# Kernel optimization log

Hardware: AMD Instinct MI355X
Metric: run time of the kernel (lower is better)

The kernel has to match this reference:

```python
import jax, jax.numpy as jnp
import numpy as np
import math

B, S, D = 2, 2048, 1024
H, DK = 16, 64
NUM_BUCKETS = 32
MAX_DISTANCE = 128


def setup_inputs() -> dict:
    key = jax.random.key(0)
    ks = jax.random.split(key, 6)
    scale = 1.0 / math.sqrt(D)
    return {
        "hidden_states": jax.random.normal(ks[0], (B, S, D), jnp.float32),
        "wq": jax.random.normal(ks[1], (D, H * DK), jnp.float32) * scale,
        "wk": jax.random.normal(ks[2], (D, H * DK), jnp.float32) * scale,
        "wv": jax.random.normal(ks[3], (D, H * DK), jnp.float32) * scale,
        "wo": jax.random.normal(ks[4], (H * DK, D), jnp.float32) * scale,
        "rel_bias": jax.random.normal(ks[5], (NUM_BUCKETS, H), jnp.float32),
    }


def _relative_position_bucket(relative_position):
    # Encoder (bidirectional) bucketing, matching T5/UMT5.
    num_buckets = NUM_BUCKETS // 2  # 16
    relative_buckets = (relative_position > 0).astype(jnp.int32) * num_buckets
    relative_position = jnp.abs(relative_position)
    max_exact = num_buckets // 2  # 8
    is_small = relative_position < max_exact
    rp_f = jnp.maximum(relative_position.astype(jnp.float32), 1.0)  # avoid log(0); masked by is_small
    log_ratio = jnp.log(rp_f / max_exact) / math.log(MAX_DISTANCE / max_exact)
    rp_large = max_exact + (log_ratio * (num_buckets - max_exact)).astype(jnp.int32)
    rp_large = jnp.minimum(rp_large, num_buckets - 1)
    return relative_buckets + jnp.where(is_small, relative_position, rp_large)


def compute_bias(query_length, key_length, rel_bias):
    ctx = jnp.arange(query_length)[:, None]
    mem = jnp.arange(key_length)[None, :]
    buckets = _relative_position_bucket(mem - ctx)  # [Sq, Sk]
    values = rel_bias[buckets]                       # [Sq, Sk, H]
    return jnp.transpose(values, (2, 0, 1))[None]    # [1, H, Sq, Sk]


def reference(hidden_states, wq, wk, wv, wo, rel_bias):
    b, s, _ = hidden_states.shape
    q = (hidden_states @ wq).reshape(b, s, H, DK).transpose(0, 2, 1, 3)  # [B,H,S,DK]
    k = (hidden_states @ wk).reshape(b, s, H, DK).transpose(0, 2, 1, 3)
    v = (hidden_states @ wv).reshape(b, s, H, DK).transpose(0, 2, 1, 3)
    scores = jnp.einsum("bhqd,bhkd->bhqk", q, k)  # no 1/sqrt(d) scaling (T5 style)
    scores = scores + compute_bias(s, s, rel_bias)
    attn = jax.nn.softmax(scores.astype(jnp.float32), axis=-1).astype(scores.dtype)
    ctx = jnp.einsum("bhqk,bhkd->bhqd", attn, v)
    ctx = ctx.transpose(0, 2, 1, 3).reshape(b, s, H * DK)
    attn_output = ctx @ wo
    return attn_output, attn
```

## Files before the change

### kernel.cpp

```cpp
#include <hip/hip_runtime.h>

typedef __attribute__((ext_vector_type(8))) short bf16x8;
typedef __attribute__((ext_vector_type(4))) float f32x4;

#define MFMA16 __builtin_amdgcn_mfma_f32_16x16x32_bf16

__device__ __forceinline__ float fexp2(float x) {
#if __has_builtin(__builtin_amdgcn_exp2f)
    return __builtin_amdgcn_exp2f(x);
#else
    return __expf(x * 0.6931471805599453f);
#endif
}

__device__ __forceinline__ short f2bf(float f) {
    union { float f; unsigned u; } v; v.f = f;
    unsigned r = v.u + 0x7fffu + ((v.u >> 16) & 1u);
    return (short)(r >> 16);
}

__device__ __forceinline__ void gl_lds16(const short* g, short* l) {
    __builtin_amdgcn_global_load_lds(
        (const __attribute__((address_space(1))) unsigned int*)g,
        (__attribute__((address_space(3))) unsigned int*)l, 16, 0, 0);
}

__global__ __launch_bounds__(256) void cast_hidden(const float* __restrict__ src,
                                                   short* __restrict__ dst, int n) {
    int i = (blockIdx.x * 256 + threadIdx.x) * 4;
    if (i < n) {
        float4 f = *(const float4*)(src + i);
        short4 o = make_short4(f2bf(f.x), f2bf(f.y), f2bf(f.z), f2bf(f.w));
        *(short4*)(dst + i) = o;
    }
}

__global__ __launch_bounds__(256) void transpose_cast(const float* __restrict__ src,
                                                      short* __restrict__ dst) {
    __shared__ float tile[32][33];
    int tx = threadIdx.x, ty = threadIdx.y;
    int bx = blockIdx.x * 32, by = blockIdx.y * 32;
#pragma unroll
    for (int i = 0; i < 4; ++i)
        tile[ty + i * 8][tx] = src[(size_t)(by + ty + i * 8) * 1024 + bx + tx];
    __syncthreads();
#pragma unroll
    for (int i = 0; i < 4; ++i)
        dst[(size_t)(bx + ty + i * 8) * 1024 + by + tx] = f2bf(tile[tx][ty + i * 8]);
}

__global__ __launch_bounds__(256) void build_bias(const float* __restrict__ relb,
                                                  float* __restrict__ tab) {
    int d = blockIdx.x * 256 + threadIdx.x;
    if (d < 4095) {
        int rel = d - 2047;
        int rp = rel < 0 ? -rel : rel;
        int bucket;
        if (rp < 8)
            bucket = rp;
        else
            bucket = 8 + (rp >= 12) + (rp >= 16) + (rp >= 23) + (rp >= 32) +
                     (rp >= 46) + (rp >= 64) + (rp >= 91);
        if (rel > 0) bucket += 16;
#pragma unroll
        for (int hh = 0; hh < 16; ++hh)
            tab[hh * 4095 + d] = relb[bucket * 16 + hh] * 1.4426950408889634f;
    }
}

__global__ __launch_bounds__(256) void gemm128(const short* __restrict__ A,
                                               const short* __restrict__ BT, int Kdim,
                                               int mode, short* __restrict__ qb,
                                               short* __restrict__ kb,
                                               short* __restrict__ vtb,
                                               float* __restrict__ fout) {
    __shared__ short As[128 * 32];
    __shared__ short Bs[128 * 32];
    const int tid = threadIdx.x, wave = tid >> 6, lane = tid & 63;
    const int quad = lane >> 4, col = lane & 15;
    const int wm = wave >> 1, wn = wave & 1;
    const int m0 = blockIdx.x * 128, n0 = blockIdx.y * 128;

    f32x4 zero4 = {0.f, 0.f, 0.f, 0.f};
    f32x4 acc[4][4];
#pragma unroll
    for (int i = 0; i < 4; ++i)
#pragma unroll
        for (int j = 0; j < 4; ++j) acc[i][j] = zero4;

    const int nk = Kdim >> 5;
    for (int kk = 0; kk < nk; ++kk) {
        __syncthreads();
#pragma unroll
        for (int c = 0; c < 2; ++c) {
            int L = c * 256 + wave * 64 + lane;
            int row = L >> 2, c4 = L & 3;
            int gc = c4 ^ ((row >> 1) & 3);
            gl_lds16(A + (size_t)(m0 + row) * Kdim + kk * 32 + gc * 8,
                     &As[(c * 256 + wave * 64) * 8]);
            gl_lds16(BT + (size_t)(n0 + row) * Kdim + kk * 32 + gc * 8,
                     &Bs[(c * 256 + wave * 64) * 8]);
        }
        __syncthreads();
        bf16x8 af[4], bfr[4];
#pragma unroll
        for (int i = 0; i < 4; ++i) {
            int ra = wm * 64 + i * 16 + col;
            af[i] = *(const bf16x8*)(&As[ra * 32 + (quad ^ ((ra >> 1) & 3)) * 8]);
            int rb = wn * 64 + i * 16 + col;
            bfr[i] = *(const bf16x8*)(&Bs[rb * 32 + (quad ^ ((rb >> 1) & 3)) * 8]);
        }
#pragma unroll
        for (int mi = 0; mi < 4; ++mi)
#pragma unroll
            for (int ni = 0; ni < 4; ++ni)
                acc[mi][ni] = MFMA16(af[mi], bfr[ni], acc[mi][ni], 0, 0, 0);
    }

#pragma unroll
    for (int mi = 0; mi < 4; ++mi) {
#pragma unroll
        for (int ni = 0; ni < 4; ++ni) {
#pragma unroll
            for (int r = 0; r < 4; ++r) {
                int gm = m0 + wm * 64 + mi * 16 + quad * 4 + r;
                int gn = n0 + wn * 64 + ni * 16 + col;
                float v = acc[mi][ni][r];
                if (mode == 1) {
                    fout[(size_t)gm * 1024 + gn] = v;
                } else {
                    int widx = gn >> 10, nn = gn & 1023;
                    int hh = nn >> 6, dk = nn & 63;
                    int bb = gm >> 11, ss = gm & 2047;
                    size_t bh = (size_t)(bb * 16 + hh);
                    if (widx == 0)
                        qb[(bh * 2048 + ss) * 64 + dk] = f2bf(v);
                    else if (widx == 1)
                        kb[(bh * 2048 + ss) * 64 + dk] = f2bf(v);
                    else
                        vtb[(bh * 64 + dk) * 2048 + ss] = f2bf(v);
                }
            }
        }
    }
}

__global__ __launch_bounds__(256) void attn_kernel(const short* __restrict__ qbuf,
                                                   const short* __restrict__ kbuf,
                                                   const short* __restrict__ vtbuf,
                                                   const float* __restrict__ bias_tab,
                                                   float* __restrict__ attn_out,
                                                   short* __restrict__ ctxbuf) {
    __shared__ short Ks[128 * 64];
    __shared__ short Vts[64 * 128];
    __shared__ short Pt[4][640];

    const int tid = threadIdx.x;
    const int wave = tid >> 6, lane = tid & 63;
    const int quad = lane >> 4, col = lane & 15;

    const int raw = blockIdx.x;
    const int blk = (raw & 7) * 128 + (raw >> 3);
    const int qt = blk & 31, h = (blk >> 5) & 15, b = blk >> 9;
    const int q0 = qt * 64 + wave * 16;

    const size_t bh = (size_t)(b * 16 + h);
    const short* Kh = kbuf + bh * 2048 * 64;
    const short* VTh = vtbuf + bh * 64 * 2048;
    const short* Qh = qbuf + bh * 2048 * 64;
    const float* btab = bias_tab + h * 4095;
    const float L2E = 1.4426950408889634f;

    bf16x8 aq0 = *(const bf16x8*)(Qh + (q0 + col) * 64 + quad * 8);
    bf16x8 aq1 = *(const bf16x8*)(Qh + (q0 + col) * 64 + 32 + quad * 8);

    float m = -1e30f, l = 0.f;

    {
#pragma unroll
        for (int c = 0; c < 4; ++c) {
            int L = c * 256 + wave * 64 + lane;
            int row = L >> 3, gc = (L & 7) ^ (row & 7);
            gl_lds16(Kh + (size_t)row * 64 + gc * 8, &Ks[(c * 256 + wave * 64) * 8]);
        }
        for (int kt = 0; kt < 16; ++kt) {
            __syncthreads();
            short* cur = (kt & 1) ? Vts : Ks;
            if (kt < 15) {
                short* nxt = (kt & 1) ? Ks : Vts;
#pragma unroll
                for (int c = 0; c < 4; ++c) {
                    int L = c * 256 + wave * 64 + lane;
                    int row = L >> 3, gc = (L & 7) ^ (row & 7);
                    gl_lds16(Kh + (size_t)((kt + 1) * 128 + row) * 64 + gc * 8,
                             &nxt[(c * 256 + wave * 64) * 8]);
                }
            }
            const float* bp = btab + (kt * 128 - (q0 + col) + 2047 + quad * 4);
            float sv[32];
            __builtin_amdgcn_s_setprio(1);
#pragma unroll
            for (int st = 0; st < 8; ++st) {
                f32x4 acc = {0.f, 0.f, 0.f, 0.f};
                int krow = st * 16 + col;
                bf16x8 bk0 = *(const bf16x8*)(&cur[krow * 64 + (quad ^ (krow & 7)) * 8]);
                bf16x8 bk1 = *(const bf16x8*)(&cur[krow * 64 + ((4 + quad) ^ (krow & 7)) * 8]);
                acc = MFMA16(bk0, aq0, acc, 0, 0, 0);
                acc = MFMA16(bk1, aq1, acc, 0, 0, 0);
#pragma unroll
                for (int r = 0; r < 4; ++r)
                    sv[st * 4 + r] = fmaf(acc[r], L2E, bp[st * 16 + r]);
            }
            __builtin_amdgcn_s_setprio(0);
            float tm = sv[0];
#pragma unroll
            for (int i = 1; i < 32; ++i) tm = fmaxf(tm, sv[i]);
            float mn = fmaxf(m, tm);
            float sum = 0.f;
#pragma unroll
            for (int i = 0; i < 32; ++i) sum += fexp2(sv[i] - mn);
            l = l * fexp2(m - mn) + sum;
            m = mn;
        }
    }
#pragma unroll
    for (int off = 16; off < 64; off <<= 1) {
        float mo = __shfl_xor(m, off);
        float lo = __shfl_xor(l, off);
        float mn = fmaxf(m, mo);
        l = l * fexp2(m - mn) + lo * fexp2(mo - mn);
        m = mn;
    }
    const float moff = m + __log2f(l);

    f32x4 zero4 = {0.f, 0.f, 0.f, 0.f};
    f32x4 ctx[4];
#pragma unroll
    for (int dt = 0; dt < 4; ++dt) ctx[dt] = zero4;

    for (int kt = 0; kt < 16; ++kt) {
        __syncthreads();
#pragma unroll
        for (int c = 0; c < 4; ++c) {
            int L = c * 256 + wave * 64 + lane;
            int row = L >> 3, gc = (L & 7) ^ (row & 7);
            gl_lds16(Kh + (size_t)(kt * 128 + row) * 64 + gc * 8,
                     &Ks[(c * 256 + wave * 64) * 8]);
        }
#pragma unroll
        for (int c = 0; c < 4; ++c) {
            int L = c * 256 + wave * 64 + lane;
            int row = L >> 4, gc = (L & 15) ^ (row & 7);
            gl_lds16(VTh + (size_t)row * 2048 + kt * 128 + gc * 8,
                     &Vts[(c * 256 + wave * 64) * 8]);
        }
        __syncthreads();
        const float* bp = btab + (kt * 128 - (q0 + col) + 2047 + quad * 4);
        float* aout = attn_out + ((bh * 2048 + q0 + col) * 2048 + kt * 128 + quad * 4);
        __builtin_amdgcn_s_setprio(1);
#pragma unroll
        for (int pr = 0; pr < 4; ++pr) {
#pragma unroll
            for (int hf = 0; hf < 2; ++hf) {
                int st = pr * 2 + hf;
                f32x4 acc = {0.f, 0.f, 0.f, 0.f};
                int krow = st * 16 + col;
                bf16x8 bk0 = *(const bf16x8*)(&Ks[krow * 64 + (quad ^ (krow & 7)) * 8]);
                bf16x8 bk1 = *(const bf16x8*)(&Ks[krow * 64 + ((4 + quad) ^ (krow & 7)) * 8]);
                acc = MFMA16(bk0, aq0, acc, 0, 0, 0);
                acc = MFMA16(bk1, aq1, acc, 0, 0, 0);
                f32x4 pv;
                short4 pb;
#pragma unroll
                for (int r = 0; r < 4; ++r) {
                    float p = fexp2(fmaf(acc[r], L2E, bp[st * 16 + r]) - moff);
                    pv[r] = p;
                    ((short*)&pb)[r] = f2bf(p);
                }
                __builtin_nontemporal_store(pv, (f32x4*)(aout + st * 16));
                *(short4*)(&Pt[wave][col * 40 + hf * 16 + quad * 4]) = pb;
            }
            bf16x8 ap = *(const bf16x8*)(&Pt[wave][col * 40 + quad * 8]);
#pragma unroll
            for (int dt = 0; dt < 4; ++dt) {
                int vrow = dt * 16 + col;
                bf16x8 bv = *(const bf16x8*)(&Vts[vrow * 128 + ((pr * 4 + quad) ^ (vrow & 7)) * 8]);
                ctx[dt] = MFMA16(ap, bv, ctx[dt], 0, 0, 0);
            }
        }
        __builtin_amdgcn_s_setprio(0);
    }
#pragma unroll
    for (int dt = 0; dt < 4; ++dt)
#pragma unroll
        for (int r = 0; r < 4; ++r) {
            int q = q0 + quad * 4 + r;
            ctxbuf[((size_t)(b * 2048 + q)) * 1024 + h * 64 + dt * 16 + col] =
                f2bf(ctx[dt][r]);
        }
}

extern "C" void kernel_launch(void* const* d_in, const int* in_sizes, int n_in,
                              void* d_out, int out_size, void* d_ws, size_t ws_size,
                              hipStream_t stream) {
    const float* hs = (const float*)d_in[0];
    const float* wq = (const float*)d_in[1];
    const float* wk = (const float*)d_in[2];
    const float* wv = (const float*)d_in[3];
    const float* wo = (const float*)d_in[4];
    const float* rb = (const float*)d_in[5];
    float* out = (float*)d_out;

    char* ws = (char*)d_ws;
    short* hsb  = (short*)(ws);
    short* wt   = (short*)(ws + ((size_t)8 << 20));
    short* wot  = (short*)(ws + ((size_t)14 << 20));
    short* qb   = (short*)(ws + ((size_t)16 << 20));
    short* kb   = (short*)(ws + ((size_t)24 << 20));
    short* vtb  = (short*)(ws + ((size_t)32 << 20));
    short* ctxb = (short*)(ws + ((size_t)40 << 20));
    float* btab = (float*)(ws + ((size_t)48 << 20));

    cast_hidden<<<4096, 256, 0, stream>>>(hs, hsb, 4096 * 1024);
    dim3 tb(32, 8);
    transpose_cast<<<dim3(32, 32), tb, 0, stream>>>(wq, wt);
    transpose_cast<<<dim3(32, 32), tb, 0, stream>>>(wk, wt + (1u << 20));
    transpose_cast<<<dim3(32, 32), tb, 0, stream>>>(wv, wt + (2u << 20));
    transpose_cast<<<dim3(32, 32), tb, 0, stream>>>(wo, wot);
    build_bias<<<16, 256, 0, stream>>>(rb, btab);

    gemm128<<<dim3(32, 24), 256, 0, stream>>>(hsb, wt, 1024, 0, qb, kb, vtb, nullptr);
    attn_kernel<<<1024, 256, 0, stream>>>(qb, kb, vtb, btab, out + 4194304, ctxb);
    gemm128<<<dim3(32, 8), 256, 0, stream>>>(ctxb, wot, 1024, 1, nullptr, nullptr, nullptr, out);
}
```

Before: 795.1 us.

## Read K/V directly from global memory and drop running-max softmax pass

Removes the LDS staging of K and V^T tiles, including the double-buffered async loads and block barriers. Each wave now loads its MFMA operands straight from global memory and relies on the cache for reuse. The first pass also drops the online max tracking and accumulates exp2 sums without subtracting a max. That saves the max reduction and rescaling, but it can overflow if scores get large. Direct global loads cost more memory traffic and latency in exchange for no synchronisation.

```diff
diff --git a/kernel.cpp b/kernel.cpp
--- a/kernel.cpp
+++ b/kernel.cpp
@@ -151,8 +151,6 @@
                                                    const float* __restrict__ bias_tab,
                                                    float* __restrict__ attn_out,
                                                    short* __restrict__ ctxbuf) {
-    __shared__ short Ks[128 * 64];
-    __shared__ short Vts[64 * 128];
     __shared__ short Pt[4][640];
 
     const int tid = threadIdx.x;
@@ -174,64 +172,26 @@
     bf16x8 aq0 = *(const bf16x8*)(Qh + (q0 + col) * 64 + quad * 8);
     bf16x8 aq1 = *(const bf16x8*)(Qh + (q0 + col) * 64 + 32 + quad * 8);
 
-    float m = -1e30f, l = 0.f;
-
-    {
-#pragma unroll
-        for (int c = 0; c < 4; ++c) {
-            int L = c * 256 + wave * 64 + lane;
-            int row = L >> 3, gc = (L & 7) ^ (row & 7);
-            gl_lds16(Kh + (size_t)row * 64 + gc * 8, &Ks[(c * 256 + wave * 64) * 8]);
-        }
-        for (int kt = 0; kt < 16; ++kt) {
-            __syncthreads();
-            short* cur = (kt & 1) ? Vts : Ks;
-            if (kt < 15) {
-                short* nxt = (kt & 1) ? Ks : Vts;
-#pragma unroll
-                for (int c = 0; c < 4; ++c) {
-                    int L = c * 256 + wave * 64 + lane;
-                    int row = L >> 3, gc = (L & 7) ^ (row & 7);
-                    gl_lds16(Kh + (size_t)((kt + 1) * 128 + row) * 64 + gc * 8,
-                             &nxt[(c * 256 + wave * 64) * 8]);
-                }
-            }
-            const float* bp = btab + (kt * 128 - (q0 + col) + 2047 + quad * 4);
-            float sv[32];
-            __builtin_amdgcn_s_setprio(1);
-#pragma unroll
-            for (int st = 0; st < 8; ++st) {
-                f32x4 acc = {0.f, 0.f, 0.f, 0.f};
-                int krow = st * 16 + col;
-                bf16x8 bk0 = *(const bf16x8*)(&cur[krow * 64 + (quad ^ (krow & 7)) * 8]);
-                bf16x8 bk1 = *(const bf16x8*)(&cur[krow * 64 + ((4 + quad) ^ (krow & 7)) * 8]);
-                acc = MFMA16(bk0, aq0, acc, 0, 0, 0);
-                acc = MFMA16(bk1, aq1, acc, 0, 0, 0);
-#pragma unroll
-                for (int r = 0; r < 4; ++r)
-                    sv[st * 4 + r] = fmaf(acc[r], L2E, bp[st * 16 + r]);
-            }
-            __builtin_amdgcn_s_setprio(0);
-            float tm = sv[0];
-#pragma unroll
-            for (int i = 1; i < 32; ++i) tm = fmaxf(tm, sv[i]);
-            float mn = fmaxf(m, tm);
-            float sum = 0.f;
-#pragma unroll
-            for (int i = 0; i < 32; ++i) sum += fexp2(sv[i] - mn);
-            l = l * fexp2(m - mn) + sum;
-            m = mn;
-        }
-    }
-#pragma unroll
-    for (int off = 16; off < 64; off <<= 1) {
-        float mo = __shfl_xor(m, off);
-        float lo = __shfl_xor(l, off);
-        float mn = fmaxf(m, mo);
-        l = l * fexp2(m - mn) + lo * fexp2(mo - mn);
-        m = mn;
-    }
-    const float moff = m + __log2f(l);
+    float l = 0.f;
+    for (int kt = 0; kt < 16; ++kt) {
+        const short* Kt = Kh + kt * 128 * 64;
+        const float* bp = btab + (kt * 128 - (q0 + col) + 2047 + quad * 4);
+#pragma unroll
+        for (int st = 0; st < 8; ++st) {
+            int krow = st * 16 + col;
+            bf16x8 bk0 = *(const bf16x8*)(Kt + krow * 64 + quad * 8);
+            bf16x8 bk1 = *(const bf16x8*)(Kt + krow * 64 + 32 + quad * 8);
+            f32x4 acc = {0.f, 0.f, 0.f, 0.f};
+            acc = MFMA16(bk0, aq0, acc, 0, 0, 0);
+            acc = MFMA16(bk1, aq1, acc, 0, 0, 0);
+#pragma unroll
+            for (int r = 0; r < 4; ++r)
+                l += fexp2(fmaf(acc[r], L2E, bp[st * 16 + r]));
+        }
+    }
+    l += __shfl_xor(l, 16);
+    l += __shfl_xor(l, 32);
+    const float moff = __log2f(l);
 
     f32x4 zero4 = {0.f, 0.f, 0.f, 0.f};
     f32x4 ctx[4];
@@ -239,22 +199,8 @@
     for (int dt = 0; dt < 4; ++dt) ctx[dt] = zero4;
 
     for (int kt = 0; kt < 16; ++kt) {
-        __syncthreads();
-#pragma unroll
-        for (int c = 0; c < 4; ++c) {
-            int L = c * 256 + wave * 64 + lane;
-            int row = L >> 3, gc = (L & 7) ^ (row & 7);
-            gl_lds16(Kh + (size_t)(kt * 128 + row) * 64 + gc * 8,
-                     &Ks[(c * 256 + wave * 64) * 8]);
-        }
-#pragma unroll
-        for (int c = 0; c < 4; ++c) {
-            int L = c * 256 + wave * 64 + lane;
-            int row = L >> 4, gc = (L & 15) ^ (row & 7);
-            gl_lds16(VTh + (size_t)row * 2048 + kt * 128 + gc * 8,
-                     &Vts[(c * 256 + wave * 64) * 8]);
-        }
-        __syncthreads();
+        const short* Kt = Kh + kt * 128 * 64;
+        const short* Vt = VTh + kt * 128;
         const float* bp = btab + (kt * 128 - (q0 + col) + 2047 + quad * 4);
         float* aout = attn_out + ((bh * 2048 + q0 + col) * 2048 + kt * 128 + quad * 4);
         __builtin_amdgcn_s_setprio(1);
@@ -263,10 +209,10 @@
 #pragma unroll
             for (int hf = 0; hf < 2; ++hf) {
                 int st = pr * 2 + hf;
+                int krow = st * 16 + col;
+                bf16x8 bk0 = *(const bf16x8*)(Kt + krow * 64 + quad * 8);
+                bf16x8 bk1 = *(const bf16x8*)(Kt + krow * 64 + 32 + quad * 8);
                 f32x4 acc = {0.f, 0.f, 0.f, 0.f};
-                int krow = st * 16 + col;
-                bf16x8 bk0 = *(const bf16x8*)(&Ks[krow * 64 + (quad ^ (krow & 7)) * 8]);
-                bf16x8 bk1 = *(const bf16x8*)(&Ks[krow * 64 + ((4 + quad) ^ (krow & 7)) * 8]);
                 acc = MFMA16(bk0, aq0, acc, 0, 0, 0);
                 acc = MFMA16(bk1, aq1, acc, 0, 0, 0);
                 f32x4 pv;
@@ -284,7 +230,7 @@
 #pragma unroll
             for (int dt = 0; dt < 4; ++dt) {
                 int vrow = dt * 16 + col;
-                bf16x8 bv = *(const bf16x8*)(&Vts[vrow * 128 + ((pr * 4 + quad) ^ (vrow & 7)) * 8]);
+                bf16x8 bv = *(const bf16x8*)(Vt + (size_t)vrow * 2048 + (pr * 4 + quad) * 8);
                 ctx[dt] = MFMA16(ap, bv, ctx[dt], 0, 0, 0);
             }
         }
```

After: 935.7 us. 17.7% more time.
